# Kernel tuning notes

Hardware: AMD Instinct MI355X
Metric: run time of the kernel (lower is better)

The kernel has to match this reference:

```python
import jax, jax.numpy as jnp
import numpy as np

N_HEAD, D_MODEL, D_K, D_V = 16, 1024, 64, 64
B, S = 4, 2048


def setup_inputs() -> dict:
    key = jax.random.key(0)
    ks = jax.random.split(key, 11)
    s = 0.02
    return {
        "q": jax.random.normal(ks[0], (B, S, D_MODEL), jnp.float32),
        "k": jax.random.normal(ks[1], (B, S, D_MODEL), jnp.float32),
        "v": jax.random.normal(ks[2], (B, S, D_MODEL), jnp.float32),
        "Wq": jax.random.normal(ks[3], (D_MODEL, N_HEAD * D_K), jnp.float32) * s,
        "bq": jnp.zeros((N_HEAD * D_K,), jnp.float32),
        "Wk": jax.random.normal(ks[4], (D_MODEL, N_HEAD * D_K), jnp.float32) * s,
        "bk": jnp.zeros((N_HEAD * D_K,), jnp.float32),
        "Wv": jax.random.normal(ks[5], (D_MODEL, N_HEAD * D_V), jnp.float32) * s,
        "bv": jnp.zeros((N_HEAD * D_V,), jnp.float32),
        "Wo": jax.random.normal(ks[6], (N_HEAD * D_V, D_MODEL), jnp.float32) * s,
        "bo": jnp.zeros((D_MODEL,), jnp.float32),
    }


def reference(q, k, v, Wq, bq, Wk, bk, Wv, bv, Wo, bo):
    b, s, _ = q.shape
    # project and split heads: [B,S,H,Dk] -> [B,H,S,Dk]
    qh = (q @ Wq + bq).reshape(b, s, N_HEAD, D_K).transpose(0, 2, 1, 3)
    kh = (k @ Wk + bk).reshape(b, s, N_HEAD, D_K).transpose(0, 2, 1, 3)
    vh = (v @ Wv + bv).reshape(b, s, N_HEAD, D_V).transpose(0, 2, 1, 3)
    scale = 1.0 / jnp.sqrt(jnp.float32(D_K))
    scores = jnp.einsum("bhqd,bhkd->bhqk", qh, kh) * scale  # [B,H,S,S]
    atten = jax.nn.softmax(scores, axis=-1)
    out = jnp.einsum("bhqk,bhkd->bhqd", atten, vh)  # [B,H,S,Dv]
    out = out.transpose(0, 2, 1, 3).reshape(b, s, N_HEAD * D_V)
    return out @ Wo + bo
```

## Files before the change

### kernel.cpp

```cpp
#include <hip/hip_runtime.h>

typedef unsigned short u16;
typedef __attribute__((ext_vector_type(4))) float f32x4;
typedef __attribute__((ext_vector_type(16))) float f32x16;
typedef __attribute__((ext_vector_type(8))) short bf16x8;
typedef __attribute__((ext_vector_type(4))) u16 u16x4;
typedef __attribute__((ext_vector_type(8))) u16 u16x8;

#define MFMA16(a, b, c) __builtin_amdgcn_mfma_f32_16x16x32_bf16((a), (b), (c), 0, 0, 0)
#define MFMA32(a, b, c) __builtin_amdgcn_mfma_f32_32x32x16_bf16((a), (b), (c), 0, 0, 0)

__device__ __forceinline__ u16 f2bf(float f) {
  union { float f; unsigned u; } x; x.f = f;
  unsigned r = x.u + 0x7fffu + ((x.u >> 16) & 1u);
  return (u16)(r >> 16);
}

__device__ __forceinline__ unsigned cvtpk(float lo, float hi) {
  unsigned r;
  asm("v_cvt_pk_bf16_f32 %0, %1, %2" : "=v"(r) : "v"(lo), "v"(hi));
  return r;
}

__device__ __forceinline__ void gl_lds16(const void* g, void* l) {
  __builtin_amdgcn_global_load_lds((const __attribute__((address_space(1))) void*)g,
                                   (__attribute__((address_space(3))) void*)l,
                                   16, 0, 0);
}

__global__ __launch_bounds__(256) void cvtT_k(const float* __restrict__ W0, const float* __restrict__ W1,
                                              const float* __restrict__ W2, const float* __restrict__ W3,
                                              u16* __restrict__ T0, u16* __restrict__ T1,
                                              u16* __restrict__ T2, u16* __restrict__ T3) {
  __shared__ u16 t[64][72];
  const float* W; u16* T;
  switch (blockIdx.z) {
    case 0: W = W0; T = T0; break;
    case 1: W = W1; T = T1; break;
    case 2: W = W2; T = T2; break;
    default: W = W3; T = T3; break;
  }
  const int tid = threadIdx.x;
  const int tr = blockIdx.x, tc = blockIdx.y;
#pragma unroll
  for (int i = 0; i < 4; ++i) {
    int row = i * 16 + (tid >> 4);
    int c4 = tid & 15;
    float4 v = *(const float4*)&W[(size_t)(tr * 64 + row) * 1024 + tc * 64 + c4 * 4];
    t[row][c4 * 4 + 0] = f2bf(v.x);
    t[row][c4 * 4 + 1] = f2bf(v.y);
    t[row][c4 * 4 + 2] = f2bf(v.z);
    t[row][c4 * 4 + 3] = f2bf(v.w);
  }
  __syncthreads();
#pragma unroll
  for (int i = 0; i < 4; ++i) {
    int orow = i * 16 + (tid >> 4);
    int occ = tid & 15;
    u16x4 o;
#pragma unroll
    for (int j = 0; j < 4; ++j) o[j] = t[occ * 4 + j][orow];
    *(u16x4*)&T[(size_t)(tc * 64 + orow) * 1024 + tr * 64 + occ * 4] = o;
  }
}

__global__ __launch_bounds__(512) void gemm_qkv_k(const float* __restrict__ Xq, const float* __restrict__ Xk,
                                                  const float* __restrict__ Xv, const u16* __restrict__ WTb,
                                                  const float* __restrict__ bq, const float* __restrict__ bk,
                                                  const float* __restrict__ bv,
                                                  u16* __restrict__ Qh, u16* __restrict__ Kh,
                                                  u16* __restrict__ Vt, float qscale) {
  __shared__ u16 As[2][128 * 64];
  __shared__ u16 Bs[2][128 * 64];
  const int tid = threadIdx.x;
  const int lane = tid & 63;
  const int w = tid >> 6;
  const int which = blockIdx.y >> 3;
  const int m0 = blockIdx.x * 128;
  const int n0 = (blockIdx.y & 7) * 128;
  const float* X = which == 0 ? Xq : (which == 1 ? Xk : Xv);
  const u16* WT = WTb + (size_t)which * 1024 * 1024;
  const float* bias = which == 0 ? bq : (which == 1 ? bk : bv);
  const int wr = (w >> 2) * 64;
  const int wc = (w & 3) * 32;
  const int l15 = lane & 15, l4 = lane >> 4, l7 = lane & 7;
  const int sr = lane >> 3;
  const int sc8 = ((lane & 7) ^ sr) * 8;
  const int arow = tid >> 3;
  const int ac = tid & 7;
  const int aswz = (ac ^ (arow & 7)) * 8;
  f32x4 acc[4][2] = {};
  float4 va_a[4], va_b[4];

#define BSTAGE(slot_, ks_) do {                                                              \
    int k0_ = (ks_) * 64;                                                                    \
    gl_lds16(WT + (size_t)(n0 + w * 16 + sr) * 1024 + k0_ + sc8, &Bs[slot_][(w * 16) * 64]);       \
    gl_lds16(WT + (size_t)(n0 + w * 16 + 8 + sr) * 1024 + k0_ + sc8, &Bs[slot_][(w * 16 + 8) * 64]); \
  } while (0)

#define ALOAD(VA, ks_) do {                                                                  \
    int k0_ = (ks_) * 64;                                                                    \
    VA[0] = *(const float4*)&X[(size_t)(m0 + arow) * 1024 + k0_ + ac * 8];                   \
    VA[1] = *(const float4*)&X[(size_t)(m0 + arow) * 1024 + k0_ + ac * 8 + 4];               \
    VA[2] = *(const float4*)&X[(size_t)(m0 + 64 + arow) * 1024 + k0_ + ac * 8];              \
    VA[3] = *(const float4*)&X[(size_t)(m0 + 64 + arow) * 1024 + k0_ + ac * 8 + 4];          \
  } while (0)

#define AWRITE(VA, slot_) do {                                                               \
    _Pragma("unroll")                                                                        \
    for (int i_ = 0; i_ < 2; ++i_) {                                                         \
      int row_ = i_ * 64 + arow;                                                             \
      const float4 vlo = VA[2 * i_], vhi = VA[2 * i_ + 1];                                   \
      u16x8 o_;                                                                              \
      o_[0] = f2bf(vlo.x); o_[1] = f2bf(vlo.y); o_[2] = f2bf(vlo.z); o_[3] = f2bf(vlo.w);    \
      o_[4] = f2bf(vhi.x); o_[5] = f2bf(vhi.y); o_[6] = f2bf(vhi.z); o_[7] = f2bf(vhi.w);    \
      *(u16x8*)&As[slot_][row_ * 64 + aswz] = o_;                                            \
    }                                                                                        \
  } while (0)

#define COMPUTE(slot_) do {                                                                  \
    const u16* Ac_ = As[slot_];                                                              \
    const u16* Bc_ = Bs[slot_];                                                              \
    _Pragma("unroll")                                                                        \
    for (int kk = 0; kk < 2; ++kk) {                                                         \
      int cs_ = ((kk * 4 + l4) ^ l7) * 8;                                                    \
      bf16x8 a_[4], b_[2];                                                                   \
      _Pragma("unroll")                                                                      \
      for (int t = 0; t < 4; ++t)                                                            \
        a_[t] = *(const bf16x8*)&Ac_[(wr + t * 16 + l15) * 64 + cs_];                        \
      _Pragma("unroll")                                                                      \
      for (int u = 0; u < 2; ++u)                                                            \
        b_[u] = *(const bf16x8*)&Bc_[(wc + u * 16 + l15) * 64 + cs_];                        \
      _Pragma("unroll")                                                                      \
      for (int mi = 0; mi < 4; ++mi)                                                         \
        _Pragma("unroll")                                                                    \
        for (int ni = 0; ni < 2; ++ni)                                                       \
          acc[mi][ni] = MFMA16(a_[mi], b_[ni], acc[mi][ni]);                                 \
    }                                                                                        \
  } while (0)

#define BODY(ks_, VA, DO_B, DO_A, VM4) do {                                                  \
    AWRITE(VA, (ks_) & 1);                                                                   \
    asm volatile("s_waitcnt lgkmcnt(0)" ::: "memory");                                       \
    if (VM4) asm volatile("s_waitcnt vmcnt(4)" ::: "memory");                                \
    else     asm volatile("s_waitcnt vmcnt(0)" ::: "memory");                                \
    __builtin_amdgcn_s_barrier();                                                            \
    if (DO_B) BSTAGE(((ks_) + 1) & 1, (ks_) + 1);                                            \
    if (DO_A) ALOAD(VA, (ks_) + 2);                                                          \
    __builtin_amdgcn_sched_barrier(0);                                                       \
    COMPUTE((ks_) & 1);                                                                      \
  } while (0)

  BSTAGE(0, 0);
  ALOAD(va_a, 0);
  ALOAD(va_b, 1);

  for (int i = 0; i < 7; ++i) {
    BODY(2 * i, va_a, 1, 1, 1);
    BODY(2 * i + 1, va_b, 1, 1, 1);
  }
  BODY(14, va_a, 1, 0, 1);
  BODY(15, va_b, 0, 0, 0);

#undef BSTAGE
#undef ALOAD
#undef AWRITE
#undef COMPUTE
#undef BODY

  const int lr = (lane >> 4) * 4;
  const int lc = lane & 15;
  if (which <= 1) {
    u16* ob = which == 0 ? Qh : Kh;
    float scale = which == 0 ? qscale : 1.0f;
#pragma unroll
    for (int mi = 0; mi < 4; ++mi)
#pragma unroll
      for (int ni = 0; ni < 2; ++ni) {
        int n = n0 + wc + ni * 16 + lc;
        float bb = bias[n];
        int h = n >> 6, d = n & 63;
#pragma unroll
        for (int r = 0; r < 4; ++r) {
          int m = m0 + wr + mi * 16 + lr + r;
          int b = m >> 11, s = m & 2047;
          ob[(((size_t)(b * 16 + h) * 2048 + s) << 6) + d] = f2bf((acc[mi][ni][r] + bb) * scale);
        }
      }
  } else {
#pragma unroll
    for (int mi = 0; mi < 4; ++mi)
#pragma unroll
      for (int ni = 0; ni < 2; ++ni) {
        int n = n0 + wc + ni * 16 + lc;
        float bb = bias[n];
        int h = n >> 6, d = n & 63;
        int m = m0 + wr + mi * 16 + lr;
        int b = m >> 11, s = m & 2047;
        u16x4 pk;
#pragma unroll
        for (int r = 0; r < 4; ++r) pk[r] = f2bf(acc[mi][ni][r] + bb);
        *(u16x4*)&Vt[((size_t)(b * 16 + h) * 64 + d) * 2048 + s] = pk;
      }
  }
}

__global__ __launch_bounds__(256) void gemm_o_k(const u16* __restrict__ X, const u16* __restrict__ WT,
                                                const float* __restrict__ bias, float* __restrict__ out) {
  __shared__ u16 As[128 * 64];
  __shared__ u16 Bs[128 * 64];
  const int tid = threadIdx.x;
  const int lane = tid & 63;
  const int w = tid >> 6;
  const int m0 = blockIdx.x * 128;
  const int n0 = blockIdx.y * 128;
  const int wr = (w >> 1) * 64;
  const int wc = (w & 1) * 64;
  const int l15 = lane & 15, l4 = lane >> 4, l7 = lane & 7;
  const int sr = lane >> 3;
  const int sc8 = ((lane & 7) ^ sr) * 8;
  f32x4 acc[4][4] = {};

  for (int ks = 0; ks < 16; ++ks) {
    const int k0 = ks * 64;
#pragma unroll
    for (int j = 0; j < 4; ++j) {
      int rb = w * 32 + j * 8;
      gl_lds16(X + (size_t)(m0 + rb + sr) * 1024 + k0 + sc8, &As[rb * 64]);
      gl_lds16(WT + (size_t)(n0 + rb + sr) * 1024 + k0 + sc8, &Bs[rb * 64]);
    }
    __syncthreads();
#pragma unroll
    for (int kk = 0; kk < 2; ++kk) {
      int cs = ((kk * 4 + l4) ^ l7) * 8;
      bf16x8 a[4], b[4];
#pragma unroll
      for (int t = 0; t < 4; ++t) {
        a[t] = *(const bf16x8*)&As[(wr + t * 16 + l15) * 64 + cs];
        b[t] = *(const bf16x8*)&Bs[(wc + t * 16 + l15) * 64 + cs];
      }
#pragma unroll
      for (int mi = 0; mi < 4; ++mi)
#pragma unroll
        for (int ni = 0; ni < 4; ++ni)
          acc[mi][ni] = MFMA16(a[mi], b[ni], acc[mi][ni]);
    }
    __syncthreads();
  }

  const int lr = (lane >> 4) * 4;
  const int lc = lane & 15;
#pragma unroll
  for (int mi = 0; mi < 4; ++mi)
#pragma unroll
    for (int ni = 0; ni < 4; ++ni) {
      int n = n0 + wc + ni * 16 + lc;
      float bb = bias[n];
#pragma unroll
      for (int r = 0; r < 4; ++r) {
        int m = m0 + wr + mi * 16 + lr + r;
        out[(size_t)m * 1024 + n] = acc[mi][ni][r] + bb;
      }
    }
}

__global__ __launch_bounds__(512) void attn_k(const u16* __restrict__ Qh, const u16* __restrict__ Kh,
                                              const u16* __restrict__ Vt, u16* __restrict__ AO) {
  __shared__ u16 SMEM[4 * 8192];
  const int lane = threadIdx.x & 63, w = threadIdx.x >> 6;
  const int hi = lane >> 5, q = lane & 31;

  const int id = blockIdx.x;
  const int bh = ((id >> 3) & 7) * 8 + (id & 7);
  const int qt = id >> 6;
  const int q0 = qt * 256 + w * 32;

  const u16* Qb = Qh + (size_t)bh * 2048 * 64;
  const u16* Kb = Kh + (size_t)bh * 2048 * 64;
  const u16* Vb = Vt + (size_t)bh * 64 * 2048;

  bf16x8 qf[4];
#pragma unroll
  for (int c = 0; c < 4; ++c)
    qf[c] = *(const bf16x8*)&Qb[(size_t)(q0 + q) * 64 + c * 16 + hi * 8];

  bf16x8 onesf;
#pragma unroll
  for (int i = 0; i < 8; ++i) onesf[i] = (short)0x3F80;

  f32x16 o0 = {}, o1 = {}, ol = {};
  const int lo8 = lane * 8;

  const int srowK = (w & 1) * 32 + q;
  const int sck = ((w >> 1) * 2 + hi) * 8;

#define STAGE(slot_, kt_) do {                                                       \
    int k0_ = (kt_) * 64;                                                            \
    gl_lds16(Kb + (size_t)(k0_ + srowK) * 64 + sck, &SMEM[(slot_) * 8192 + w * 512]);          \
    gl_lds16(Vb + (size_t)srowK * 2048 + k0_ + sck, &SMEM[(slot_) * 8192 + 4096 + w * 512]);   \
  } while (0)

  STAGE(0, 0);
  STAGE(1, 1);
  STAGE(2, 2);

  for (int kt = 0; kt < 32; ++kt) {
    if (kt < 30)       asm volatile("s_waitcnt vmcnt(4)" ::: "memory");
    else if (kt == 30) asm volatile("s_waitcnt vmcnt(2)" ::: "memory");
    else               asm volatile("s_waitcnt vmcnt(0)" ::: "memory");
    __builtin_amdgcn_s_barrier();
    if (kt <= 28) STAGE((kt + 3) & 3, kt + 3);
    __builtin_amdgcn_sched_barrier(0);

    const u16* Kc = &SMEM[(kt & 3) * 8192];
    const u16* Vc = Kc + 4096;

    f32x16 s0 = {}, s1 = {};
    __builtin_amdgcn_s_setprio(1);
#pragma unroll
    for (int c = 0; c < 4; ++c) {
      bf16x8 k0 = *(const bf16x8*)&Kc[(c * 2) * 512 + lo8];
      bf16x8 k1 = *(const bf16x8*)&Kc[(c * 2 + 1) * 512 + lo8];
      s0 = MFMA32(k0, qf[c], s0);
      s1 = MFMA32(k1, qf[c], s1);
    }
    __builtin_amdgcn_s_setprio(0);

#pragma unroll
    for (int i = 0; i < 16; ++i) {
      s0[i] = __builtin_exp2f(s0[i]);
      s1[i] = __builtin_exp2f(s1[i]);
    }

    __builtin_amdgcn_s_setprio(1);
#pragma unroll
    for (int t = 0; t < 4; ++t) {
      unsigned wA, wB, wC, wD;
      if (t == 0) { wA = cvtpk(s0[0], s0[1]); wB = cvtpk(s0[2], s0[3]); wC = cvtpk(s0[4], s0[5]); wD = cvtpk(s0[6], s0[7]); }
      else if (t == 1) { wA = cvtpk(s0[8], s0[9]); wB = cvtpk(s0[10], s0[11]); wC = cvtpk(s0[12], s0[13]); wD = cvtpk(s0[14], s0[15]); }
      else if (t == 2) { wA = cvtpk(s1[0], s1[1]); wB = cvtpk(s1[2], s1[3]); wC = cvtpk(s1[4], s1[5]); wD = cvtpk(s1[6], s1[7]); }
      else { wA = cvtpk(s1[8], s1[9]); wB = cvtpk(s1[10], s1[11]); wC = cvtpk(s1[12], s1[13]); wD = cvtpk(s1[14], s1[15]); }
      asm("v_permlane32_swap_b32 %0, %1" : "+v"(wA), "+v"(wC));
      asm("v_permlane32_swap_b32 %0, %1" : "+v"(wB), "+v"(wD));
      union { unsigned u[4]; bf16x8 v; } pf;
      pf.u[0] = wA; pf.u[1] = wB; pf.u[2] = wC; pf.u[3] = wD;
      bf16x8 v0 = *(const bf16x8*)&Vc[(t * 2) * 512 + lo8];
      bf16x8 v1 = *(const bf16x8*)&Vc[(t * 2 + 1) * 512 + lo8];
      o0 = MFMA32(v0, pf.v, o0);
      o1 = MFMA32(v1, pf.v, o1);
      ol = MFMA32(onesf, pf.v, ol);
    }
    __builtin_amdgcn_s_setprio(0);
  }
#undef STAGE

  __builtin_amdgcn_s_barrier();

  float inv = 1.0f / ol[0];
  u16* ep = SMEM + w * 2048;
#pragma unroll
  for (int g = 0; g < 2; ++g) {
    const f32x16 oo = g ? o1 : o0;
#pragma unroll
    for (int j = 0; j < 8; ++j) {
      int d = g * 32 + (j & 1) * 2 + ((j >> 1) & 1) * 8 + (j >> 2) * 16 + 4 * hi;
      unsigned pw = cvtpk(oo[2 * j] * inv, oo[2 * j + 1] * inv);
      *(unsigned*)&ep[q * 64 + ((d >> 3) ^ (q & 7)) * 8 + (d & 7)] = pw;
    }
  }
  asm volatile("s_waitcnt lgkmcnt(0)" ::: "memory");
  const int b = bh >> 4, h = bh & 15;
#pragma unroll
  for (int i = 0; i < 4; ++i) {
    int r = i * 8 + (lane >> 3), c = lane & 7;
    u16x8 vv = *(const u16x8*)&ep[r * 64 + ((c ^ (r & 7)) * 8)];
    size_t row = (size_t)b * 2048 + q0 + r;
    *(u16x8*)&AO[row * 1024 + h * 64 + c * 8] = vv;
  }
}

extern "C" void kernel_launch(void* const* d_in, const int* in_sizes, int n_in,
                              void* d_out, int out_size, void* d_ws, size_t ws_size,
                              hipStream_t stream) {
  const float* q  = (const float*)d_in[0];
  const float* k  = (const float*)d_in[1];
  const float* v  = (const float*)d_in[2];
  const float* Wq = (const float*)d_in[3];
  const float* bq = (const float*)d_in[4];
  const float* Wk = (const float*)d_in[5];
  const float* bk = (const float*)d_in[6];
  const float* Wv = (const float*)d_in[7];
  const float* bv = (const float*)d_in[8];
  const float* Wo = (const float*)d_in[9];
  const float* bo = (const float*)d_in[10];
  float* out = (float*)d_out;

  char* ws = (char*)d_ws;
  const size_t SZX = (size_t)8192 * 1024 * 2;
  const size_t SZW = (size_t)1024 * 1024 * 2;
  u16* AO  = (u16*)(ws);
  u16* WTq = (u16*)(ws + 3 * SZX);
  u16* WTk = (u16*)(ws + 3 * SZX + SZW);
  u16* WTv = (u16*)(ws + 3 * SZX + 2 * SZW);
  u16* WTo = (u16*)(ws + 3 * SZX + 3 * SZW);
  u16* Qh  = (u16*)(ws + 3 * SZX + 4 * SZW);
  u16* Kh  = (u16*)(ws + 4 * SZX + 4 * SZW);
  u16* Vt  = (u16*)(ws + 5 * SZX + 4 * SZW);

  cvtT_k<<<dim3(16, 16, 4), dim3(256), 0, stream>>>(Wq, Wk, Wv, Wo, WTq, WTk, WTv, WTo);

  gemm_qkv_k<<<dim3(64, 24), dim3(512), 0, stream>>>(q, k, v, WTq, bq, bk, bv, Qh, Kh, Vt,
                                                     0.125f * 1.4426950408889634f);

  attn_k<<<dim3(512), dim3(512), 0, stream>>>(Qh, Kh, Vt, AO);

  gemm_o_k<<<dim3(64, 8), dim3(256), 0, stream>>>(AO, WTo, bo, out);
}
```

Measured before the change: 196.7 us.

## Triple-buffer weight tiles in QKV GEMM and use packed bf16 conversion

The B (weight) tile in the QKV projection GEMM is staged two k-steps ahead through a third LDS buffer, so global-to-LDS weight loads get more time to land before use. The A tile fp32-to-bf16 conversion now uses the packed hardware convert instruction instead of a manual rounding per element. The extra buffer raises LDS use per block, which may lower occupancy. The fixed vmcnt(6) wait also covers the final iterations where no new loads are issued, so those steps may wait more loosely than needed or rely on the counter semantics.

```diff
diff --git a/kernel.cpp b/kernel.cpp
--- a/kernel.cpp
+++ b/kernel.cpp
@@ -71,7 +71,7 @@
                                                   u16* __restrict__ Qh, u16* __restrict__ Kh,
                                                   u16* __restrict__ Vt, float qscale) {
   __shared__ u16 As[2][128 * 64];
-  __shared__ u16 Bs[2][128 * 64];
+  __shared__ u16 Bs[3][128 * 64];
   const int tid = threadIdx.x;
   const int lane = tid & 63;
   const int w = tid >> 6;
@@ -111,16 +111,16 @@
     for (int i_ = 0; i_ < 2; ++i_) {                                                         \
       int row_ = i_ * 64 + arow;                                                             \
       const float4 vlo = VA[2 * i_], vhi = VA[2 * i_ + 1];                                   \
-      u16x8 o_;                                                                              \
-      o_[0] = f2bf(vlo.x); o_[1] = f2bf(vlo.y); o_[2] = f2bf(vlo.z); o_[3] = f2bf(vlo.w);    \
-      o_[4] = f2bf(vhi.x); o_[5] = f2bf(vhi.y); o_[6] = f2bf(vhi.z); o_[7] = f2bf(vhi.w);    \
-      *(u16x8*)&As[slot_][row_ * 64 + aswz] = o_;                                            \
+      union { unsigned u[4]; u16x8 v; } o_;                                                  \
+      o_.u[0] = cvtpk(vlo.x, vlo.y); o_.u[1] = cvtpk(vlo.z, vlo.w);                          \
+      o_.u[2] = cvtpk(vhi.x, vhi.y); o_.u[3] = cvtpk(vhi.z, vhi.w);                          \
+      *(u16x8*)&As[slot_][row_ * 64 + aswz] = o_.v;                                          \
     }                                                                                        \
   } while (0)
 
-#define COMPUTE(slot_) do {                                                                  \
-    const u16* Ac_ = As[slot_];                                                              \
-    const u16* Bc_ = Bs[slot_];                                                              \
+#define COMPUTE(aslot_, bslot_) do {                                                         \
+    const u16* Ac_ = As[aslot_];                                                             \
+    const u16* Bc_ = Bs[bslot_];                                                             \
     _Pragma("unroll")                                                                        \
     for (int kk = 0; kk < 2; ++kk) {                                                         \
       int cs_ = ((kk * 4 + l4) ^ l7) * 8;                                                    \
@@ -139,28 +139,27 @@
     }                                                                                        \
   } while (0)
 
-#define BODY(ks_, VA, DO_B, DO_A, VM4) do {                                                  \
+#define BODY(ks_, VA, DO_NEXT) do {                                                          \
     AWRITE(VA, (ks_) & 1);                                                                   \
     asm volatile("s_waitcnt lgkmcnt(0)" ::: "memory");                                       \
-    if (VM4) asm volatile("s_waitcnt vmcnt(4)" ::: "memory");                                \
-    else     asm volatile("s_waitcnt vmcnt(0)" ::: "memory");                                \
+    asm volatile("s_waitcnt vmcnt(6)" ::: "memory");         \
     __builtin_amdgcn_s_barrier();                                                            \
-    if (DO_B) BSTAGE(((ks_) + 1) & 1, (ks_) + 1);                                            \
-    if (DO_A) ALOAD(VA, (ks_) + 2);                                                          \
+    if (DO_NEXT) { BSTAGE(((ks_) + 2) % 3, (ks_) + 2); ALOAD(VA, (ks_) + 2); }               \
     __builtin_amdgcn_sched_barrier(0);                                                       \
-    COMPUTE((ks_) & 1);                                                                      \
+    COMPUTE((ks_) & 1, (ks_) % 3);                                                           \
   } while (0)
 
   BSTAGE(0, 0);
+  BSTAGE(1, 1);
   ALOAD(va_a, 0);
   ALOAD(va_b, 1);
 
   for (int i = 0; i < 7; ++i) {
-    BODY(2 * i, va_a, 1, 1, 1);
-    BODY(2 * i + 1, va_b, 1, 1, 1);
-  }
-  BODY(14, va_a, 1, 0, 1);
-  BODY(15, va_b, 0, 0, 0);
+    BODY(2 * i, va_a, 1);
+    BODY(2 * i + 1, va_b, 1);
+  }
+  BODY(14, va_a, 0);
+  BODY(15, va_b, 0);
 
 #undef BSTAGE
 #undef ALOAD
```

Measured after the change: 195.7 us. About the same (-0.5%).
